# Optimization experiments

Hardware: AMD Instinct MI355X
Metric: run time of the kernel (lower is better)

## Reference

```python
import jax, jax.numpy as jnp
import numpy as np
import math

TOPK = 32

def setup_inputs() -> dict:
    key = jax.random.key(0)
    k1, k2, k3, k4 = jax.random.split(key, 4)
    B, D_e, D_o, T, H, W = 2, 128, 256, 16, 64, 64
    H_ref = W_ref = 32  # resolution_ref = 2
    THW_ref = T * H_ref * W_ref
    HW_ref = H_ref * W_ref
    return {
        "m_in": jax.random.normal(k1, (B, D_e, T, H, W), jnp.float32),
        "m_out": jax.random.normal(k2, (B, D_o, T, H, W), jnp.float32),
        "q_in": jax.random.normal(k3, (B, D_e, H, W), jnp.float32),
        "qk_ref": jax.random.normal(k4, (B, THW_ref, HW_ref), jnp.float32),
    }


def reference(m_in, m_out, q_in, qk_ref):
    B, D_e, T, H, W = m_in.shape
    D_o = m_out.shape[1]
    _, THW_ref, HW_ref = qk_ref.shape
    res = int(math.sqrt(H * W // HW_ref))
    H_ref, W_ref = H // res, W // res
    s = res
    k = TOPK

    # top-k memory blocks for each of the HW_ref query blocks
    topk_val, topk_idx = jax.lax.top_k(jnp.swapaxes(qk_ref, 1, 2), k)  # [B, HW_ref, k]
    # torch path scatters one-hot then uses nonzero -> gather order is ascending-index;
    # softmax-attention over n is permutation invariant, but sort for exact faithfulness.
    idx_sorted = jnp.sort(topk_idx, axis=-1)

    def blockify(m, D):
        # [B,D,T,H,W] -> [B, T*H_ref*W_ref, s, s, D]
        m = m.reshape(B, D, T, H_ref, s, W_ref, s)
        m = m.transpose(0, 2, 3, 5, 4, 6, 1)  # B,T,H_ref,W_ref,s,s,D
        return m.reshape(B, T * H_ref * W_ref, s, s, D)

    m_in_b = blockify(m_in, D_e)
    m_out_b = blockify(m_out, D_o)

    flat_idx = idx_sorted.reshape(B, HW_ref * k)
    gather = jax.vmap(lambda mb, i: mb[i])  # per-batch fancy gather of blocks
    m_in_sel = gather(m_in_b, flat_idx).reshape(B, H_ref, W_ref, k * s * s, D_e)
    m_out_sel = gather(m_out_b, flat_idx).reshape(B, H_ref, W_ref, k * s * s, D_o)

    # query blocks: [B, H_ref, W_ref, D_e, s, s]
    q = q_in.reshape(B, D_e, H_ref, s, W_ref, s).transpose(0, 2, 4, 1, 3, 5)

    p = jnp.einsum('bhwnc,bhwcij->bhwijn', m_in_sel, q) / math.sqrt(D_e)
    p = jax.nn.softmax(p, axis=-1)
    mem_out = jnp.einsum('bhwnc,bhwijn->bchiwj', m_out_sel, p).reshape(B, D_o, H, W)

    kk = max(k // 4, 1)
    return mem_out, topk_idx[:, :, :kk], topk_val[:, :, :kk]
```

## Files before the change

### kernel.cpp

```cpp
#include <hip/hip_runtime.h>
#include <math.h>



__device__ inline unsigned mono_u32(float f) {
    unsigned b = __float_as_uint(f);
    return (b & 0x80000000u) ? ~b : (b | 0x80000000u);
}

__global__ __launch_bounds__(256) void qk_chunk_max(const float* __restrict__ qk,
                                                    float* __restrict__ Mx) {
    int wg = blockIdx.x;
    int chunk = wg & 127;
    int b = wg >> 7;
    int tid = threadIdx.x;
    const float4* p = (const float4*)(qk + ((size_t)b * 16384 + (size_t)chunk * 128) * 1024) + tid;
    float4 m4;
    m4.x = m4.y = m4.z = m4.w = -__builtin_inff();
#pragma unroll
    for (int rb = 0; rb < 16; ++rb) {
        float4 v[8];
#pragma unroll
        for (int u = 0; u < 8; ++u)
            v[u] = p[(size_t)(rb * 8 + u) * 256];
#pragma unroll
        for (int u = 0; u < 8; ++u) {
            m4.x = fmaxf(m4.x, v[u].x); m4.y = fmaxf(m4.y, v[u].y);
            m4.z = fmaxf(m4.z, v[u].z); m4.w = fmaxf(m4.w, v[u].w);
        }
    }
    ((float4*)Mx)[(size_t)wg * 256 + tid] = m4;
}

__global__ __launch_bounds__(256) void qk_thresh(const float* __restrict__ Mx,
                                                 unsigned* __restrict__ t_u,
                                                 int* __restrict__ cnt) {
    int g = blockIdx.x * 256 + threadIdx.x;
    if (g < 2048) cnt[g] = 0;
    int colg = blockIdx.x * 4 + (threadIdx.x >> 6);
    int lane = threadIdx.x & 63;
    int b = colg >> 10, col = colg & 1023;
    const float* base = Mx + (size_t)b * 131072 + col;
    float v0 = base[(size_t)lane * 1024];
    float v1 = base[(size_t)(lane + 64) * 1024];
    unsigned long long k0 = ((unsigned long long)mono_u32(v0) << 32) | (unsigned)lane;
    unsigned long long k1 = ((unsigned long long)mono_u32(v1) << 32) | (unsigned)(lane + 64);
    int r0 = 0, r1 = 0;
#pragma unroll 8
    for (int j = 0; j < 64; ++j) {
        unsigned long long o0 = __shfl(k0, j, 64);
        unsigned long long o1 = __shfl(k1, j, 64);
        r0 += (o0 > k0) ? 1 : 0; r0 += (o1 > k0) ? 1 : 0;
        r1 += (o0 > k1) ? 1 : 0; r1 += (o1 > k1) ? 1 : 0;
    }
    if (r0 == 31) t_u[colg] = (unsigned)(k0 >> 32);
    if (r1 == 31) t_u[colg] = (unsigned)(k1 >> 32);
}

__global__ __launch_bounds__(256) void qk_filter(const float* __restrict__ qk,
                                                 const unsigned* __restrict__ t_u,
                                                 int* __restrict__ cnt,
                                                 unsigned long long* __restrict__ cand) {
    int wg = blockIdx.x;
    int chunk = wg & 127;
    int b = wg >> 7;
    int tid = threadIdx.x;
    const float4* p = (const float4*)(qk + ((size_t)b * 16384 + (size_t)chunk * 128) * 1024) + tid;
    uint4 tu = ((const uint4*)t_u)[b * 256 + tid];
    int colg0 = b * 1024 + 4 * tid;
#pragma unroll
    for (int rb = 0; rb < 16; ++rb) {
        float4 v[8];
#pragma unroll
        for (int u = 0; u < 8; ++u)
            v[u] = p[(size_t)(rb * 8 + u) * 256];
#pragma unroll
        for (int u = 0; u < 8; ++u) {
            int row = chunk * 128 + rb * 8 + u;
            unsigned ux = mono_u32(v[u].x), uy = mono_u32(v[u].y);
            unsigned uz = mono_u32(v[u].z), uw = mono_u32(v[u].w);
            if (ux >= tu.x) {
                int pos = atomicAdd(&cnt[colg0 + 0], 1);
                if (pos < 256) cand[(size_t)(colg0 + 0) * 256 + pos] =
                    ((unsigned long long)ux << 32) | (unsigned long long)(16383 - row);
            }
            if (uy >= tu.y) {
                int pos = atomicAdd(&cnt[colg0 + 1], 1);
                if (pos < 256) cand[(size_t)(colg0 + 1) * 256 + pos] =
                    ((unsigned long long)uy << 32) | (unsigned long long)(16383 - row);
            }
            if (uz >= tu.z) {
                int pos = atomicAdd(&cnt[colg0 + 2], 1);
                if (pos < 256) cand[(size_t)(colg0 + 2) * 256 + pos] =
                    ((unsigned long long)uz << 32) | (unsigned long long)(16383 - row);
            }
            if (uw >= tu.w) {
                int pos = atomicAdd(&cnt[colg0 + 3], 1);
                if (pos < 256) cand[(size_t)(colg0 + 3) * 256 + pos] =
                    ((unsigned long long)uw << 32) | (unsigned long long)(16383 - row);
            }
        }
    }
}

__global__ __launch_bounds__(256) void topk_select(const unsigned long long* __restrict__ cand,
                                                   const int* __restrict__ cnt,
                                                   const float* __restrict__ qk,
                                                   float* __restrict__ out_idx,
                                                   float* __restrict__ out_val,
                                                   int* __restrict__ idx_sorted) {
    int bid = blockIdx.x;
    int tid = threadIdx.x;
    __shared__ unsigned long long sc[256];
    __shared__ unsigned long long selk[32];

    int C = cnt[bid];
    if (C <= 256) {
        if (tid < C) sc[tid] = cand[(size_t)bid * 256 + tid];
        __syncthreads();
        if (tid < C) {
            unsigned long long mine = sc[tid];
            int rank = 0;
            for (int j = 0; j < C; ++j) rank += (sc[j] > mine) ? 1 : 0;
            if (rank < 32) selk[rank] = mine;
        }
        __syncthreads();
    } else {
        int b = bid >> 10, q = bid & 1023;
        const float* colp = qk + (size_t)b * 16384 * 1024 + q;
        unsigned long long prev = ~0ull;
#pragma unroll 1
        for (int s = 0; s < 32; ++s) {
            unsigned long long best = 0;
            for (int r = tid; r < 16384; r += 256) {
                unsigned long long k =
                    ((unsigned long long)mono_u32(colp[(size_t)r * 1024]) << 32) |
                    (unsigned long long)(16383 - r);
                if (k < prev && k > best) best = k;
            }
            sc[tid] = best;
            __syncthreads();
            for (int off = 128; off >= 1; off >>= 1) {
                if (tid < off && sc[tid + off] > sc[tid]) sc[tid] = sc[tid + off];
                __syncthreads();
            }
            if (tid == 0) selk[s] = sc[0];
            __syncthreads();
            prev = selk[s];
        }
    }

    if (tid < 8) {
        unsigned long long k = selk[tid];
        unsigned uv = (unsigned)(k >> 32);
        unsigned bits = (uv & 0x80000000u) ? (uv ^ 0x80000000u) : ~uv;
        out_val[(size_t)bid * 8 + tid] = __uint_as_float(bits);
        int gi = 16383 - (int)(k & 0xFFFFFFFFull);
        out_idx[(size_t)bid * 8 + tid] = (float)gi;
    }
    if (tid < 32) {
        int mine = 16383 - (int)(selk[tid] & 0xFFFFFFFFull);
        int rank = 0;
#pragma unroll
        for (int j = 0; j < 32; ++j) {
            int oj = 16383 - (int)(selk[j] & 0xFFFFFFFFull);
            rank += (oj < mine) ? 1 : 0;
        }
        idx_sorted[(size_t)bid * 32 + rank] = mine;
    }
}

template <int D, int T>
__global__ __launch_bounds__(256) void blockify2(const float* __restrict__ in,
                                                 float* __restrict__ out) {
    constexpr int NH = D / 128;
    __shared__ float tile[128][128];
    int wg = blockIdx.x;
    int h  = wg % NH;
    int hb = (wg / NH) % 32;
    int t  = (wg / (NH * 32)) % T;
    int b  = wg / (NH * 32 * T);
    int tid = threadIdx.x;

    {
        int m   = tid & 31;
        int cl0 = tid >> 5;
        float4 v[16];
#pragma unroll
        for (int pass = 0; pass < 16; ++pass) {
            int c = pass * 8 + cl0;
            const float* src = in +
                ((size_t)(b * D + h * 128 + c) * T + t) * 4096 + (size_t)hb * 128;
            v[pass] = *(const float4*)(src + 4 * m);
        }
#pragma unroll
        for (int pass = 0; pass < 16; ++pass) {
            int c = pass * 8 + cl0;
            int sw = ((c >> 2) & 31) << 2;
            *(float4*)&tile[c][(4 * m) ^ sw] = v[pass];
        }
    }
    __syncthreads();

    {
        size_t slab = (((size_t)b * T + t) * 1024 + (size_t)hb * 32) * (4 * D) +
                      (size_t)h * 128;
#pragma unroll
        for (int it = 0; it < 16; ++it) {
            int flat = it * 1024 + tid * 4;
            int cl = flat & 127;
            int pp = (flat >> 7) & 3;
            int wb = flat >> 9;
            int pos = ((pp >> 1) << 6) + 2 * wb + (pp & 1);
            int sw = ((cl >> 2) & 31) << 2;
            float4 o;
            o.x = tile[cl + 0][pos ^ sw];
            o.y = tile[cl + 1][pos ^ sw];
            o.z = tile[cl + 2][pos ^ sw];
            o.w = tile[cl + 3][pos ^ sw];
            *(float4*)(out + slab + (size_t)wb * 4 * D + (size_t)pp * D + cl) = o;
        }
    }
}

__global__ __launch_bounds__(256) void attn_kernel(const float* __restrict__ m_in_b,
                                                   const float* __restrict__ m_out_b,
                                                   const float* __restrict__ q_b,
                                                   const int* __restrict__ idx_sorted,
                                                   float* __restrict__ out) {
    int bid = blockIdx.x;
    int b = bid >> 10, qblk = bid & 1023;
    int hb = qblk >> 5, wb = qblk & 31;
    int tid = threadIdx.x;
    int w = tid >> 6, lane = tid & 63;

    __shared__ float K[64][129];
    __shared__ float Q[4][128];
    __shared__ float P[4][128];
    __shared__ int   blks[32];

    if (tid < 32) blks[tid] = idx_sorted[(size_t)bid * 32 + tid];
    {
        const float* qsrc = q_b + (size_t)bid * 512;
        ((float*)Q)[tid]       = qsrc[tid];
        ((float*)Q)[tid + 256] = qsrc[tid + 256];
    }
    __syncthreads();

    const float scale = 0.08838834764831845f;
    float s01[2];
#pragma unroll 1
    for (int half = 0; half < 2; ++half) {
        if (half) __syncthreads();
#pragma unroll 4
        for (int ki = 0; ki < 16; ++ki) {
            int blk = blks[half * 16 + ki];
            const float* src = m_in_b + ((size_t)b * 16384 + blk) * 512;
            int p0 = tid >> 7, c0 = tid & 127;
            K[ki * 4 + p0][c0]     = src[tid];
            K[ki * 4 + p0 + 2][c0] = src[tid + 256];
        }
        __syncthreads();
        float acc = 0.f;
#pragma unroll 4
        for (int c = 0; c < 128; ++c) acc += K[lane][c] * Q[w][c];
        s01[half] = acc * scale;
    }

    float m = fmaxf(s01[0], s01[1]);
#pragma unroll
    for (int off = 32; off >= 1; off >>= 1) m = fmaxf(m, __shfl_xor(m, off, 64));
    float e0 = expf(s01[0] - m), e1 = expf(s01[1] - m);
    float sum = e0 + e1;
#pragma unroll
    for (int off = 32; off >= 1; off >>= 1) sum += __shfl_xor(sum, off, 64);
    float inv = 1.0f / sum;
    P[w][lane]      = e0 * inv;
    P[w][lane + 64] = e1 * inv;
    __syncthreads();

    float a0 = 0.f, a1 = 0.f, a2 = 0.f, a3 = 0.f;
    int d = tid;
#pragma unroll 1
    for (int ki = 0; ki < 32; ++ki) {
        const float* vsrc = m_out_b + ((size_t)b * 16384 + blks[ki]) * 1024;
#pragma unroll
        for (int p = 0; p < 4; ++p) {
            float vv = vsrc[p * 256 + d];
            int n = ki * 4 + p;
            a0 += P[0][n] * vv; a1 += P[1][n] * vv;
            a2 += P[2][n] * vv; a3 += P[3][n] * vv;
        }
    }
    size_t base = (((size_t)b * 256 + d) * 64 + hb * 2) * 64 + wb * 2;
    out[base]      = a0;
    out[base + 1]  = a1;
    out[base + 64] = a2;
    out[base + 65] = a3;
}

extern "C" void kernel_launch(void* const* d_in, const int* in_sizes, int n_in,
                              void* d_out, int out_size, void* d_ws, size_t ws_size,
                              hipStream_t stream) {
    const float* m_in  = (const float*)d_in[0];
    const float* m_out = (const float*)d_in[1];
    const float* q_in  = (const float*)d_in[2];
    const float* qk    = (const float*)d_in[3];

    char* ws = (char*)d_ws;
    float* m_out_b = (float*)(ws);
    float* m_in_b  = (float*)(ws + 134217728);
    float* q_b     = (float*)(ws + 201326592);
    int*   idxs    = (int*)  (ws + 205520896);

    unsigned long long* cand = (unsigned long long*)(ws);
    float*    Mx  = (float*)   (ws + 4194304);
    unsigned* t_u = (unsigned*)(ws + 5242880);
    int*      cnt = (int*)     (ws + 5251072);

    float* out     = (float*)d_out;
    float* out_mem = out;
    float* out_idx = out + 2097152;
    float* out_val = out + 2113536;

    qk_chunk_max<<<256, 256, 0, stream>>>(qk, Mx);
    qk_thresh   <<<512, 256, 0, stream>>>(Mx, t_u, cnt);
    qk_filter   <<<256, 256, 0, stream>>>(qk, t_u, cnt, cand);
    topk_select <<<2048, 256, 0, stream>>>(cand, cnt, qk, out_idx, out_val, idxs);

    blockify2<128, 16><<<1024, 256, 0, stream>>>(m_in, m_in_b);
    blockify2<128, 1><<<64, 256, 0, stream>>>(q_in, q_b);
    blockify2<256, 16><<<2048, 256, 0, stream>>>(m_out, m_out_b);
    attn_kernel<<<2048, 256, 0, stream>>>(m_in_b, m_out_b, q_b, idxs, out_mem);
}
```

Baseline: 542.6 us.

## Split top-k prefilter into finer chunks with radix-histogram threshold and bitmask filter

```diff
diff --git a/kernel.cpp b/kernel.cpp
--- a/kernel.cpp
+++ b/kernel.cpp
@@ -11,14 +11,14 @@
 __global__ __launch_bounds__(256) void qk_chunk_max(const float* __restrict__ qk,
                                                     float* __restrict__ Mx) {
     int wg = blockIdx.x;
-    int chunk = wg & 127;
-    int b = wg >> 7;
-    int tid = threadIdx.x;
-    const float4* p = (const float4*)(qk + ((size_t)b * 16384 + (size_t)chunk * 128) * 1024) + tid;
+    int chunk = wg & 511;
+    int b = wg >> 9;
+    int tid = threadIdx.x;
+    const float4* p = (const float4*)(qk + ((size_t)b * 16384 + (size_t)chunk * 32) * 1024) + tid;
     float4 m4;
     m4.x = m4.y = m4.z = m4.w = -__builtin_inff();
 #pragma unroll
-    for (int rb = 0; rb < 16; ++rb) {
+    for (int rb = 0; rb < 4; ++rb) {
         float4 v[8];
 #pragma unroll
         for (int u = 0; u < 8; ++u)
@@ -35,26 +35,73 @@
 __global__ __launch_bounds__(256) void qk_thresh(const float* __restrict__ Mx,
                                                  unsigned* __restrict__ t_u,
                                                  int* __restrict__ cnt) {
-    int g = blockIdx.x * 256 + threadIdx.x;
-    if (g < 2048) cnt[g] = 0;
-    int colg = blockIdx.x * 4 + (threadIdx.x >> 6);
-    int lane = threadIdx.x & 63;
+    int colg = blockIdx.x;
+    int tid = threadIdx.x;
     int b = colg >> 10, col = colg & 1023;
-    const float* base = Mx + (size_t)b * 131072 + col;
-    float v0 = base[(size_t)lane * 1024];
-    float v1 = base[(size_t)(lane + 64) * 1024];
-    unsigned long long k0 = ((unsigned long long)mono_u32(v0) << 32) | (unsigned)lane;
-    unsigned long long k1 = ((unsigned long long)mono_u32(v1) << 32) | (unsigned)(lane + 64);
-    int r0 = 0, r1 = 0;
-#pragma unroll 8
-    for (int j = 0; j < 64; ++j) {
-        unsigned long long o0 = __shfl(k0, j, 64);
-        unsigned long long o1 = __shfl(k1, j, 64);
-        r0 += (o0 > k0) ? 1 : 0; r0 += (o1 > k0) ? 1 : 0;
-        r1 += (o0 > k1) ? 1 : 0; r1 += (o1 > k1) ? 1 : 0;
-    }
-    if (r0 == 31) t_u[colg] = (unsigned)(k0 >> 32);
-    if (r1 == 31) t_u[colg] = (unsigned)(k1 >> 32);
+    const float* base = Mx + (size_t)b * 524288 + col;
+    unsigned u0 = mono_u32(base[(size_t)tid * 1024]);
+    unsigned u1 = mono_u32(base[(size_t)(tid + 256) * 1024]);
+
+    __shared__ int hist1[256];
+    __shared__ int hist2[256];
+    __shared__ int s_b1, s_above1;
+    __shared__ unsigned s_tu;
+    hist1[tid] = 0; hist2[tid] = 0;
+    __syncthreads();
+
+    atomicAdd(&hist1[u0 >> 24], 1);
+    atomicAdd(&hist1[u1 >> 24], 1);
+    __syncthreads();
+
+    if (tid < 64) {
+        int base4 = 252 - 4 * tid;
+        int h0 = hist1[base4], h1 = hist1[base4 + 1], h2 = hist1[base4 + 2], h3 = hist1[base4 + 3];
+        int gs = h0 + h1 + h2 + h3;
+        int pre = gs;
+#pragma unroll
+        for (int off = 1; off < 64; off <<= 1) {
+            int o = __shfl_up(pre, off, 64);
+            if (tid >= off) pre += o;
+        }
+        int excl = pre - gs;
+        if (excl < 32 && pre >= 32) {
+            int c = excl, bb, ab;
+            c += h3; if (c >= 32) { bb = base4 + 3; ab = c - h3; }
+            else { c += h2; if (c >= 32) { bb = base4 + 2; ab = c - h2; }
+            else { c += h1; if (c >= 32) { bb = base4 + 1; ab = c - h1; }
+            else { c += h0;   bb = base4;     ab = c - h0; } } }
+            s_b1 = bb; s_above1 = ab;
+        }
+    }
+    __syncthreads();
+    int b1 = s_b1;
+    if ((int)(u0 >> 24) == b1) atomicAdd(&hist2[(u0 >> 16) & 0xFF], 1);
+    if ((int)(u1 >> 24) == b1) atomicAdd(&hist2[(u1 >> 16) & 0xFF], 1);
+    __syncthreads();
+
+    if (tid < 64) {
+        int A = s_above1;
+        int base4 = 252 - 4 * tid;
+        int h0 = hist2[base4], h1 = hist2[base4 + 1], h2 = hist2[base4 + 2], h3 = hist2[base4 + 3];
+        int gs = h0 + h1 + h2 + h3;
+        int pre = gs;
+#pragma unroll
+        for (int off = 1; off < 64; off <<= 1) {
+            int o = __shfl_up(pre, off, 64);
+            if (tid >= off) pre += o;
+        }
+        int excl = pre - gs;
+        if (A + excl < 32 && A + pre >= 32) {
+            int c = A + excl, bb;
+            c += h3; if (c >= 32) bb = base4 + 3;
+            else { c += h2; if (c >= 32) bb = base4 + 2;
+            else { c += h1; if (c >= 32) bb = base4 + 1;
+            else { bb = base4; } } }
+            s_tu = (((unsigned)b1 << 8) | (unsigned)bb) << 16;
+        }
+    }
+    __syncthreads();
+    if (tid == 0) { t_u[colg] = s_tu; cnt[colg] = 0; }
 }
 
 __global__ __launch_bounds__(256) void qk_filter(const float* __restrict__ qk,
@@ -62,43 +109,45 @@
                                                  int* __restrict__ cnt,
                                                  unsigned long long* __restrict__ cand) {
     int wg = blockIdx.x;
-    int chunk = wg & 127;
-    int b = wg >> 7;
-    int tid = threadIdx.x;
-    const float4* p = (const float4*)(qk + ((size_t)b * 16384 + (size_t)chunk * 128) * 1024) + tid;
+    int chunk = wg & 511;
+    int b = wg >> 9;
+    int tid = threadIdx.x;
+    const float4* p = (const float4*)(qk + ((size_t)b * 16384 + (size_t)chunk * 32) * 1024) + tid;
     uint4 tu = ((const uint4*)t_u)[b * 256 + tid];
-    int colg0 = b * 1024 + 4 * tid;
-#pragma unroll
-    for (int rb = 0; rb < 16; ++rb) {
+
+    unsigned mxm = 0, mym = 0, mzm = 0, mwm = 0;
+#pragma unroll
+    for (int rb = 0; rb < 4; ++rb) {
         float4 v[8];
 #pragma unroll
         for (int u = 0; u < 8; ++u)
             v[u] = p[(size_t)(rb * 8 + u) * 256];
 #pragma unroll
         for (int u = 0; u < 8; ++u) {
-            int row = chunk * 128 + rb * 8 + u;
-            unsigned ux = mono_u32(v[u].x), uy = mono_u32(v[u].y);
-            unsigned uz = mono_u32(v[u].z), uw = mono_u32(v[u].w);
-            if (ux >= tu.x) {
-                int pos = atomicAdd(&cnt[colg0 + 0], 1);
-                if (pos < 256) cand[(size_t)(colg0 + 0) * 256 + pos] =
-                    ((unsigned long long)ux << 32) | (unsigned long long)(16383 - row);
-            }
-            if (uy >= tu.y) {
-                int pos = atomicAdd(&cnt[colg0 + 1], 1);
-                if (pos < 256) cand[(size_t)(colg0 + 1) * 256 + pos] =
-                    ((unsigned long long)uy << 32) | (unsigned long long)(16383 - row);
-            }
-            if (uz >= tu.z) {
-                int pos = atomicAdd(&cnt[colg0 + 2], 1);
-                if (pos < 256) cand[(size_t)(colg0 + 2) * 256 + pos] =
-                    ((unsigned long long)uz << 32) | (unsigned long long)(16383 - row);
-            }
-            if (uw >= tu.w) {
-                int pos = atomicAdd(&cnt[colg0 + 3], 1);
-                if (pos < 256) cand[(size_t)(colg0 + 3) * 256 + pos] =
-                    ((unsigned long long)uw << 32) | (unsigned long long)(16383 - row);
-            }
+            int r = rb * 8 + u;
+            mxm |= (mono_u32(v[u].x) >= tu.x ? 1u : 0u) << r;
+            mym |= (mono_u32(v[u].y) >= tu.y ? 1u : 0u) << r;
+            mzm |= (mono_u32(v[u].z) >= tu.z ? 1u : 0u) << r;
+            mwm |= (mono_u32(v[u].w) >= tu.w ? 1u : 0u) << r;
+        }
+    }
+
+    int row0 = chunk * 32;
+    int colg0 = b * 1024 + 4 * tid;
+    const float* q0 = qk + ((size_t)b * 16384 + row0) * 1024 + 4 * tid;
+    unsigned msk[4] = {mxm, mym, mzm, mwm};
+#pragma unroll
+    for (int j = 0; j < 4; ++j) {
+        unsigned m = msk[j];
+        while (m) {
+            int r = __ffs(m) - 1;
+            m &= m - 1;
+            unsigned uu = mono_u32(q0[(size_t)r * 1024 + j]);
+            int pos = atomicAdd(&cnt[colg0 + j], 1);
+            if (pos < 256)
+                cand[(size_t)(colg0 + j) * 256 + pos] =
+                    ((unsigned long long)uu << 32) |
+                    (unsigned long long)(16383 - (row0 + r));
         }
     }
 }
@@ -315,17 +364,17 @@
 
     unsigned long long* cand = (unsigned long long*)(ws);
     float*    Mx  = (float*)   (ws + 4194304);
-    unsigned* t_u = (unsigned*)(ws + 5242880);
-    int*      cnt = (int*)     (ws + 5251072);
+    unsigned* t_u = (unsigned*)(ws + 8388608);
+    int*      cnt = (int*)     (ws + 8396800);
 
     float* out     = (float*)d_out;
     float* out_mem = out;
     float* out_idx = out + 2097152;
     float* out_val = out + 2113536;
 
-    qk_chunk_max<<<256, 256, 0, stream>>>(qk, Mx);
-    qk_thresh   <<<512, 256, 0, stream>>>(Mx, t_u, cnt);
-    qk_filter   <<<256, 256, 0, stream>>>(qk, t_u, cnt, cand);
+    qk_chunk_max<<<1024, 256, 0, stream>>>(qk, Mx);
+    qk_thresh   <<<2048, 256, 0, stream>>>(Mx, t_u, cnt);
+    qk_filter   <<<1024, 256, 0, stream>>>(qk, t_u, cnt, cand);
     topk_select <<<2048, 256, 0, stream>>>(cand, cnt, qk, out_idx, out_val, idxs);
 
     blockify2<128, 16><<<1024, 256, 0, stream>>>(m_in, m_in_b);
```

New measurement: 472.2 us. 1.15x faster.
